# Kernel tuning notes

Hardware: AMD Instinct MI355X
Metric: run time of the kernel (lower is better)

Reference implementation:

```python
import jax, jax.numpy as jnp
import numpy as np

BETA_THRESH = 0.1   # threshold fraction in forward
BETA_IPOT = 0.5     # IPOT entropic beta
ITERATION = 30


def setup_inputs() -> dict:
    key = jax.random.key(0)
    k1, k2 = jax.random.split(key)
    bs, n, m, d = 64, 512, 512, 768
    return {
        "local_features_1": jax.random.normal(k1, (bs, n, d), dtype=jnp.float32),
        "local_features_2": jax.random.normal(k2, (bs, m, d), dtype=jnp.float32),
    }


def _wasserstein_loss(x, y):
    # x: (bs, n, d), y: (bs, m, d)
    # cost_matrix_batch_torch normalizes over the feature dim (dim=1 of bs*d*n layout)
    xn = x / (jnp.linalg.norm(x, axis=2, keepdims=True) + 1e-12)
    yn = y / (jnp.linalg.norm(y, axis=2, keepdims=True) + 1e-12)
    # cost_matrix returns (1 - cos).transpose(2,1); forward transposes back -> (bs, n, m)
    cos_distance = 1.0 - jnp.einsum("bnd,bmd->bnm", xn, yn)
    # global min/max threshold + relu
    min_score = cos_distance.min()
    max_score = cos_distance.max()
    threshold = min_score + BETA_THRESH * (max_score - min_score)
    C = jax.nn.relu(cos_distance - threshold)  # (bs, n, m)
    bs, n, m = C.shape
    A = jnp.exp(-C / BETA_IPOT)
    T0 = jnp.ones((bs, n, m), dtype=C.dtype)
    sigma0 = jnp.full((bs, m, 1), 1.0 / m, dtype=C.dtype)

    def step(carry, _):
        T, sigma = carry
        Q = A * T                                      # (bs, n, m)
        delta = 1.0 / (n * jnp.matmul(Q, sigma))       # (bs, n, 1)
        a = jnp.matmul(jnp.swapaxes(Q, 1, 2), delta)   # (bs, m, 1)
        sigma = 1.0 / (m * a)                          # (bs, m, 1)
        T = delta * Q * jnp.swapaxes(sigma, 1, 2)      # (bs, n, m)
        return (T, sigma), None

    (T, _), _ = jax.lax.scan(step, (T0, sigma0), None, length=ITERATION)
    # batch_trace(C^T @ T) == sum_ij C_ij * T_ij per batch element
    distance = jnp.einsum("bnm,bnm->b", C, T)
    # IPOT_distance returns -distance; loss is its mean
    return (-distance).mean()


def reference(local_features_1, local_features_2):
    return _wasserstein_loss(local_features_1, local_features_2)
```

## Files before the change

kernel.cpp:

```cpp
#include <hip/hip_runtime.h>
#include <hip/hip_fp16.h>

#define NN 512
#define DD 768

typedef _Float16 half8 __attribute__((ext_vector_type(8)));
typedef _Float16 half4 __attribute__((ext_vector_type(4)));
typedef _Float16 half2v __attribute__((ext_vector_type(2)));
typedef float f32x4 __attribute__((ext_vector_type(4)));

__device__ __forceinline__ int f2ord(float f) {
  int i = __float_as_int(f);
  return i < 0 ? (i ^ 0x7fffffff) : i;
}
__device__ __forceinline__ float ord2f(int i) {
  return __int_as_float(i < 0 ? (i ^ 0x7fffffff) : i);
}

__device__ __forceinline__ void glds16(const void* g, void* l) {
  __builtin_amdgcn_global_load_lds((const __attribute__((address_space(1))) void*)g,
                                   (__attribute__((address_space(3))) void*)l, 16, 0, 0);
}

__global__ void k_init(int* meta, int* cnt) {
  int t = threadIdx.x;
  if (t == 0) {
    meta[0] = 0x7fffffff;
    meta[1] = 0x80000000;
    cnt[1024] = 0;
  }
  if (t < 64) cnt[t * 16] = 0;
}

__global__ __launch_bounds__(256) void k_norm(const float* __restrict__ f1,
                                              const float* __restrict__ f2,
                                              __half* __restrict__ xn,
                                              __half* __restrict__ yn) {
  int row = blockIdx.x * 4 + (threadIdx.x >> 6);
  int lane = threadIdx.x & 63;
  int r = row & 32767;
  const float* src = (row < 32768 ? f1 : f2) + (size_t)r * DD;
  __half* dst = (row < 32768 ? xn : yn) + (size_t)r * DD;
  f32x4 v0 = *(const f32x4*)(src + lane * 4);
  f32x4 v1 = *(const f32x4*)(src + lane * 4 + 256);
  f32x4 v2 = *(const f32x4*)(src + lane * 4 + 512);
  float s = v0[0]*v0[0] + v0[1]*v0[1] + v0[2]*v0[2] + v0[3]*v0[3]
          + v1[0]*v1[0] + v1[1]*v1[1] + v1[2]*v1[2] + v1[3]*v1[3]
          + v2[0]*v2[0] + v2[1]*v2[1] + v2[2]*v2[2] + v2[3]*v2[3];
  #pragma unroll
  for (int m = 1; m < 64; m <<= 1) s += __shfl_xor(s, m, 64);
  float f = 1.0f / (sqrtf(s) + 1e-12f);
  union U { __half2 h2[2]; uint2 u; };
  U u0, u1, u2;
  u0.h2[0] = __floats2half2_rn(v0[0]*f, v0[1]*f); u0.h2[1] = __floats2half2_rn(v0[2]*f, v0[3]*f);
  u1.h2[0] = __floats2half2_rn(v1[0]*f, v1[1]*f); u1.h2[1] = __floats2half2_rn(v1[2]*f, v1[3]*f);
  u2.h2[0] = __floats2half2_rn(v2[0]*f, v2[1]*f); u2.h2[1] = __floats2half2_rn(v2[2]*f, v2[3]*f);
  *(uint2*)(dst + lane * 4)       = u0.u;
  *(uint2*)(dst + lane * 4 + 256) = u1.u;
  *(uint2*)(dst + lane * 4 + 512) = u2.u;
}

#define FOR16(X) X(0) X(1) X(2) X(3) X(4) X(5) X(6) X(7) X(8) X(9) X(10) X(11) X(12) X(13) X(14) X(15)

#define AGLD(p) __hip_atomic_load((p), __ATOMIC_RELAXED, __HIP_MEMORY_SCOPE_AGENT)
#define AGST(p, v) __hip_atomic_store((p), (v), __ATOMIC_RELAXED, __HIP_MEMORY_SCOPE_AGENT)

struct IpotLds {
  float xs[128];
  float ys[NN];
  _Float16 zs[NN];
  _Float16 csh[8][520];
  float wred[8];
};
union MainLds {
  _Float16 Bs[2][16384];
  _Float16 At[4][8192];
  float mm[16];
  int mmi[16];
  IpotLds ip;
};

__global__ __launch_bounds__(512, 2) void k_main(const __half* __restrict__ xn,
                                                 const __half* __restrict__ yn,
                                                 int* __restrict__ meta,
                                                 int* __restrict__ cnt,
                                                 int* __restrict__ gmm,
                                                 float* __restrict__ gpart,
                                                 float* __restrict__ gdist) {
  __shared__ __align__(16) MainLds u;
  const int blk = blockIdx.x;
  const int b = blk & 63, qq = blk >> 6;
  const int tid = threadIdx.x;
  const int sv = tid >> 6, lane = tid & 63;
  const int fr = lane & 15;
  const int g8 = (lane >> 4) * 8;
  const int r0 = sv * 16;
  const int c0 = lane * 8;
  const __half* xnb = xn + ((size_t)b * NN + qq * 128 + sv * 16) * DD;
  const __half* ynb = yn + (size_t)b * NN * DD;

  f32x4 acc[32] = {};
#define STAGE(bf, kk) { \
    const __half* ys_ = ynb + (size_t)(sv * 64 + lane) * DD + (kk); \
    glds16(ys_ +  0, (char*)u.Bs[bf] +     sv * 1024); \
    glds16(ys_ +  8, (char*)u.Bs[bf] +  8192 + sv * 1024); \
    glds16(ys_ + 16, (char*)u.Bs[bf] + 16384 + sv * 1024); \
    glds16(ys_ + 24, (char*)u.Bs[bf] + 24576 + sv * 1024); }
  int buf = 0;
  STAGE(0, 0)
  half8 afp = *(const half8*)(xnb + (size_t)fr * DD + g8);
  for (int kk = 0; kk < DD; kk += 32) {
    __syncthreads();
    if (kk + 32 < DD) STAGE(buf ^ 1, kk + 32)
    half8 afc = afp;
    if (kk + 32 < DD) afp = *(const half8*)(xnb + (size_t)fr * DD + (kk + 32) + g8);
    #pragma unroll
    for (int c = 0; c < 32; ++c) {
      half8 bf = *(const half8*)(&u.Bs[buf][(lane >> 4) * 4096 + (16 * c + fr) * 8]);
      acc[c] = __builtin_amdgcn_mfma_f32_16x16x32_f16(afc, bf, acc[c], 0, 0, 0);
    }
    buf ^= 1;
  }

  float vmin = 1e30f, vmax = -1e30f;
  #pragma unroll
  for (int c = 0; c < 32; ++c) {
    #pragma unroll
    for (int r2 = 0; r2 < 4; ++r2) {
      float val = 1.0f - acc[c][r2];
      vmin = fminf(vmin, val); vmax = fmaxf(vmax, val);
    }
  }
  #pragma unroll
  for (int m = 1; m < 64; m <<= 1) {
    vmin = fminf(vmin, __shfl_xor(vmin, m, 64));
    vmax = fmaxf(vmax, __shfl_xor(vmax, m, 64));
  }
  __syncthreads();
  if (lane == 0) { u.mm[sv] = vmin; u.mm[8 + sv] = vmax; }
  __syncthreads();
  if (tid == 0) {
    float bm = u.mm[0], bx = u.mm[8];
    #pragma unroll
    for (int g = 1; g < 8; ++g) { bm = fminf(bm, u.mm[g]); bx = fmaxf(bx, u.mm[8 + g]); }
    AGST(gmm + blk, f2ord(bm));
    AGST(gmm + 256 + blk, f2ord(bx));
  }
  __syncthreads();
  if (tid == 0) {
    int* cnt2 = cnt + 1024;
    __hip_atomic_fetch_add(cnt2, 1, __ATOMIC_RELAXED, __HIP_MEMORY_SCOPE_AGENT);
    while (AGLD(cnt2) < 256) __builtin_amdgcn_s_sleep(1);
  }
  __syncthreads();
  {
    int mo = AGLD(gmm + tid);
    #pragma unroll
    for (int m = 1; m < 64; m <<= 1) {
      int o = __shfl_xor(mo, m, 64);
      mo = (sv < 4) ? (mo < o ? mo : o) : (mo > o ? mo : o);
    }
    if (lane == 0) u.mmi[sv] = mo;
  }
  __syncthreads();
  int gmnord = u.mmi[0], gmxord = u.mmi[4];
  #pragma unroll
  for (int g = 1; g < 4; ++g) {
    gmnord = gmnord < u.mmi[g] ? gmnord : u.mmi[g];
    gmxord = gmxord > u.mmi[4 + g] ? gmxord : u.mmi[4 + g];
  }
  const float gmn = ord2f(gmnord);
  const float gmx = ord2f(gmxord);
  const float thr = gmn + 0.1f * (gmx - gmn);

#define DECLAM(r) half8 A##r, M##r;
  FOR16(DECLAM)

#define TWRITE { \
    _Float16* reg_ = u.At[sv & 3]; \
    const int q_ = lane >> 4; \
    _Pragma("unroll") \
    for (int c = 0; c < 32; ++c) { \
      _Pragma("unroll") \
      for (int r2 = 0; r2 < 4; ++r2) { \
        float val_ = 1.0f - acc[c][r2]; \
        float a_ = __expf(-2.0f * fmaxf(val_ - thr, 0.0f)); \
        int off_ = (((4 * q_ + r2) * 1024 + (16 * c + fr) * 2) ^ (q_ << 4)) >> 1; \
        reg_[off_] = (_Float16)a_; \
      } \
    } }

#define TREAD(r) { \
    A##r = *(const half8*)((const char*)u.At[sv & 3] + \
            (((r) * 1024 + lane * 16) ^ ((((r) >> 2) & 3) << 4))); \
    M##r = A##r; }

  __syncthreads();
  if (sv < 4) TWRITE
  __syncthreads();
  if (sv < 4) { FOR16(TREAD) }
  __syncthreads();
  if (sv >= 4) TWRITE
  __syncthreads();
  if (sv >= 4) { FOR16(TREAD) }
  __syncthreads();

  if (tid < 256) *(half2v*)(u.ip.zs + 2 * tid) = (half2v){(_Float16)1.0f, (_Float16)1.0f};
  u.ip.ys[tid] = 1.0f;
  __syncthreads();

  int* mycnt = cnt + b * 16;

  #pragma unroll 1
  for (int t = 1; t <= 30; ++t) {
    half8 zv = *(const half8*)(u.ip.zs + c0);
    float rp16[16];
#define ROWP(r) { \
      half8 p = M##r * zv; \
      half4 q = p.lo + p.hi; \
      half2v q2 = q.lo + q.hi; \
      rp16[r] = (float)q2.x + (float)q2.y; }
    FOR16(ROWP)
    float c8[8];
    #pragma unroll
    for (int i = 0; i < 8; ++i) {
      float keep = (lane & 1) ? rp16[2*i+1] : rp16[2*i];
      float send = (lane & 1) ? rp16[2*i]   : rp16[2*i+1];
      c8[i] = keep + __shfl_xor(send, 1, 64);
    }
    float c4[4];
    #pragma unroll
    for (int i = 0; i < 4; ++i) {
      float keep = (lane & 2) ? c8[2*i+1] : c8[2*i];
      float send = (lane & 2) ? c8[2*i]   : c8[2*i+1];
      c4[i] = keep + __shfl_xor(send, 2, 64);
    }
    float d2[2];
    #pragma unroll
    for (int i = 0; i < 2; ++i) {
      float keep = (lane & 4) ? c4[2*i+1] : c4[2*i];
      float send = (lane & 4) ? c4[2*i]   : c4[2*i+1];
      d2[i] = keep + __shfl_xor(send, 4, 64);
    }
    float c1;
    {
      float keep = (lane & 8) ? d2[1] : d2[0];
      float send = (lane & 8) ? d2[0] : d2[1];
      c1 = keep + __shfl_xor(send, 8, 64);
    }
    c1 += __shfl_xor(c1, 16, 64);
    c1 += __shfl_xor(c1, 32, 64);
    if (lane < 16) u.ip.xs[r0 + lane] = 1.0f / c1;
    half8 cac = (half8)(_Float16)0.0f;
#define COLP(r) { _Float16 xh = (_Float16)u.ip.xs[r0 + r]; cac += M##r * xh; }
    FOR16(COLP)
    *(half8*)(&u.ip.csh[sv][c0]) = cac;
#define UPDM(r) M##r *= A##r;
    if (t < 30) { FOR16(UPDM) }
    __syncthreads();
    float* gp = gpart + ((size_t)((t & 1) * 256 + blk) * 512);
    if (tid < 256) {
      float a0 = 0.0f, a1 = 0.0f;
      #pragma unroll
      for (int g = 0; g < 8; ++g) {
        half2v pv = *(const half2v*)(&u.ip.csh[g][2 * tid]);
        a0 += (float)pv.x; a1 += (float)pv.y;
      }
      AGST(gp + tid * 2,     a0);
      AGST(gp + tid * 2 + 1, a1);
    }
    __syncthreads();
    if (tid == 0) {
      __hip_atomic_fetch_add(mycnt, 1, __ATOMIC_RELAXED, __HIP_MEMORY_SCOPE_AGENT);
      while (__hip_atomic_load(mycnt, __ATOMIC_RELAXED, __HIP_MEMORY_SCOPE_AGENT) < 4 * t)
        __builtin_amdgcn_s_sleep(1);
    }
    __syncthreads();
    if (tid < 256) {
      float a0 = 0.0f, a1 = 0.0f;
      #pragma unroll
      for (int q2 = 0; q2 < 4; ++q2) {
        const float* gpb = gpart + ((size_t)((t & 1) * 256 + b + 64 * q2) * 512);
        a0 += AGLD(gpb + tid * 2);
        a1 += AGLD(gpb + tid * 2 + 1);
      }
      float yo0 = u.ip.ys[2 * tid], yo1 = u.ip.ys[2 * tid + 1];
      float y0 = 1.0f / a0;
      float y1 = 1.0f / a1;
      *(half2v*)(u.ip.zs + 2 * tid) = (half2v){(_Float16)(y0 * y0 / yo0), (_Float16)(y1 * y1 / yo1)};
      u.ip.ys[2 * tid] = y0; u.ip.ys[2 * tid + 1] = y1;
    }
    __syncthreads();
  }

  float contrib = 0.0f;
#define FINP(r) { \
    float rowacc = 0.0f; \
    rowacc += -0.34657359f * __log2f((float)A##r.s0) * (float)M##r.s0 * u.ip.ys[c0 + 0]; \
    rowacc += -0.34657359f * __log2f((float)A##r.s1) * (float)M##r.s1 * u.ip.ys[c0 + 1]; \
    rowacc += -0.34657359f * __log2f((float)A##r.s2) * (float)M##r.s2 * u.ip.ys[c0 + 2]; \
    rowacc += -0.34657359f * __log2f((float)A##r.s3) * (float)M##r.s3 * u.ip.ys[c0 + 3]; \
    rowacc += -0.34657359f * __log2f((float)A##r.s4) * (float)M##r.s4 * u.ip.ys[c0 + 4]; \
    rowacc += -0.34657359f * __log2f((float)A##r.s5) * (float)M##r.s5 * u.ip.ys[c0 + 5]; \
    rowacc += -0.34657359f * __log2f((float)A##r.s6) * (float)M##r.s6 * u.ip.ys[c0 + 6]; \
    rowacc += -0.34657359f * __log2f((float)A##r.s7) * (float)M##r.s7 * u.ip.ys[c0 + 7]; \
    contrib += rowacc * u.ip.xs[r0 + r]; }
  FOR16(FINP)
  #pragma unroll
  for (int m = 1; m < 64; m <<= 1) contrib += __shfl_xor(contrib, m, 64);
  if (lane == 0) u.ip.wred[sv] = contrib;
  __syncthreads();
  if (tid == 0) {
    float s2 = 0.0f;
    #pragma unroll
    for (int g = 0; g < 8; ++g) s2 += u.ip.wred[g];
    gdist[blk] = s2;
  }
}

__global__ void k_final(const float* __restrict__ gdist, float* __restrict__ out) {
  int b = threadIdx.x & 63;
  float v = gdist[b] + gdist[b + 64] + gdist[b + 128] + gdist[b + 192];
  #pragma unroll
  for (int m = 1; m < 64; m <<= 1) v += __shfl_xor(v, m, 64);
  if (threadIdx.x == 0) out[0] = -v * (1.0f / (64.0f * 512.0f));
}

extern "C" void kernel_launch(void* const* d_in, const int* in_sizes, int n_in,
                              void* d_out, int out_size, void* d_ws, size_t ws_size,
                              hipStream_t stream) {
  const float* f1 = (const float*)d_in[0];
  const float* f2 = (const float*)d_in[1];
  char* ws = (char*)d_ws;
  __half* xn   = (__half*)(ws + 0);
  __half* yn   = (__half*)(ws + 50331648);
  float* gpart = (float*)(ws + 100663296);
  int*   meta  = (int*)(ws + 167772160);
  int*   cnt   = (int*)(ws + 167772160 + 256);
  int*   gmm   = (int*)(ws + 167772160 + 256 + 8192);
  float* gdist = (float*)(ws + 167772160 + 256 + 8192 + 2048);

  k_init<<<1, 64, 0, stream>>>(meta, cnt);
  k_norm<<<16384, 256, 0, stream>>>(f1, f2, xn, yn);
  k_main<<<256, 512, 0, stream>>>(xn, yn, meta, cnt, gmm, gpart, gdist);
  k_final<<<1, 64, 0, stream>>>(gdist, (float*)d_out);
}
```

Baseline: 227.0 us.

## Pack cross-block IPOT partial sums as half2 and coalesce B-tile staging

The per-iteration cross-block column partial sums are now stored in global memory as packed half2 words instead of two floats, halving the traffic exchanged between cooperating blocks on each of the 30 IPOT iterations. The Y-tile staging into LDS is reorganized so that groups of four lanes read contiguous 64-byte row segments, and the LDS fragment indexing changes to match. The spin-wait loop now uses an explicit atomic load. Rounding partial sums to fp16 before the reciprocal adds precision loss to the sigma update.

```diff
diff --git a/kernel.cpp b/kernel.cpp
--- a/kernel.cpp
+++ b/kernel.cpp
@@ -85,7 +85,7 @@
                                                  int* __restrict__ meta,
                                                  int* __restrict__ cnt,
                                                  int* __restrict__ gmm,
-                                                 float* __restrict__ gpart,
+                                                 unsigned* __restrict__ gpart,
                                                  float* __restrict__ gdist) {
   __shared__ __align__(16) MainLds u;
   const int blk = blockIdx.x;
@@ -101,11 +101,11 @@
 
   f32x4 acc[32] = {};
 #define STAGE(bf, kk) { \
-    const __half* ys_ = ynb + (size_t)(sv * 64 + lane) * DD + (kk); \
-    glds16(ys_ +  0, (char*)u.Bs[bf] +     sv * 1024); \
-    glds16(ys_ +  8, (char*)u.Bs[bf] +  8192 + sv * 1024); \
-    glds16(ys_ + 16, (char*)u.Bs[bf] + 16384 + sv * 1024); \
-    glds16(ys_ + 24, (char*)u.Bs[bf] + 24576 + sv * 1024); }
+    _Pragma("unroll") \
+    for (int j = 0; j < 4; ++j) { \
+      const __half* ys_ = ynb + (size_t)(128 * j + sv * 16 + (lane >> 2)) * DD + (kk) + (lane & 3) * 8; \
+      glds16(ys_, (char*)u.Bs[bf] + j * 8192 + sv * 1024); \
+    } }
   int buf = 0;
   STAGE(0, 0)
   half8 afp = *(const half8*)(xnb + (size_t)fr * DD + g8);
@@ -116,7 +116,7 @@
     if (kk + 32 < DD) afp = *(const half8*)(xnb + (size_t)fr * DD + (kk + 32) + g8);
     #pragma unroll
     for (int c = 0; c < 32; ++c) {
-      half8 bf = *(const half8*)(&u.Bs[buf][(lane >> 4) * 4096 + (16 * c + fr) * 8]);
+      half8 bf = *(const half8*)(&u.Bs[buf][(16 * c + fr) * 32 + g8]);
       acc[c] = __builtin_amdgcn_mfma_f32_16x16x32_f16(afc, bf, acc[c], 0, 0, 0);
     }
     buf ^= 1;
@@ -143,18 +143,19 @@
     float bm = u.mm[0], bx = u.mm[8];
     #pragma unroll
     for (int g = 1; g < 8; ++g) { bm = fminf(bm, u.mm[g]); bx = fmaxf(bx, u.mm[8 + g]); }
-    AGST(gmm + blk, f2ord(bm));
-    AGST(gmm + 256 + blk, f2ord(bx));
+    AGST(gmm + blk, (unsigned)f2ord(bm));
+    AGST(gmm + 256 + blk, (unsigned)f2ord(bx));
   }
   __syncthreads();
   if (tid == 0) {
     int* cnt2 = cnt + 1024;
     __hip_atomic_fetch_add(cnt2, 1, __ATOMIC_RELAXED, __HIP_MEMORY_SCOPE_AGENT);
-    while (AGLD(cnt2) < 256) __builtin_amdgcn_s_sleep(1);
+    while (__hip_atomic_load(cnt2, __ATOMIC_RELAXED, __HIP_MEMORY_SCOPE_AGENT) < 256)
+      __builtin_amdgcn_s_sleep(1);
   }
   __syncthreads();
   {
-    int mo = AGLD(gmm + tid);
+    int mo = (int)AGLD(gmm + tid);
     #pragma unroll
     for (int m = 1; m < 64; m <<= 1) {
       int o = __shfl_xor(mo, m, 64);
@@ -258,7 +259,7 @@
 #define UPDM(r) M##r *= A##r;
     if (t < 30) { FOR16(UPDM) }
     __syncthreads();
-    float* gp = gpart + ((size_t)((t & 1) * 256 + blk) * 512);
+    unsigned* gp = gpart + ((size_t)((t & 1) * 256 + blk) * 256);
     if (tid < 256) {
       float a0 = 0.0f, a1 = 0.0f;
       #pragma unroll
@@ -266,8 +267,8 @@
         half2v pv = *(const half2v*)(&u.ip.csh[g][2 * tid]);
         a0 += (float)pv.x; a1 += (float)pv.y;
       }
-      AGST(gp + tid * 2,     a0);
-      AGST(gp + tid * 2 + 1, a1);
+      __half2 ph = __floats2half2_rn(a0, a1);
+      AGST(gp + tid, *reinterpret_cast<unsigned*>(&ph));
     }
     __syncthreads();
     if (tid == 0) {
@@ -280,9 +281,10 @@
       float a0 = 0.0f, a1 = 0.0f;
       #pragma unroll
       for (int q2 = 0; q2 < 4; ++q2) {
-        const float* gpb = gpart + ((size_t)((t & 1) * 256 + b + 64 * q2) * 512);
-        a0 += AGLD(gpb + tid * 2);
-        a1 += AGLD(gpb + tid * 2 + 1);
+        unsigned v = AGLD(gpart + ((size_t)((t & 1) * 256 + b + 64 * q2) * 256) + tid);
+        __half2 h = *reinterpret_cast<__half2*>(&v);
+        float2 fv = __half22float2(h);
+        a0 += fv.x; a1 += fv.y;
       }
       float yo0 = u.ip.ys[2 * tid], yo1 = u.ip.ys[2 * tid + 1];
       float y0 = 1.0f / a0;
@@ -334,7 +336,7 @@
   char* ws = (char*)d_ws;
   __half* xn   = (__half*)(ws + 0);
   __half* yn   = (__half*)(ws + 50331648);
-  float* gpart = (float*)(ws + 100663296);
+  unsigned* gpart = (unsigned*)(ws + 100663296);
   int*   meta  = (int*)(ws + 167772160);
   int*   cnt   = (int*)(ws + 167772160 + 256);
   int*   gmm   = (int*)(ws + 167772160 + 256 + 8192);
@@ -342,6 +344,6 @@
 
   k_init<<<1, 64, 0, stream>>>(meta, cnt);
   k_norm<<<16384, 256, 0, stream>>>(f1, f2, xn, yn);
-  k_main<<<256, 512, 0, stream>>>(xn, yn, meta, cnt, gmm, gpart, gdist);
+  k_main<<<256, 512, 0, stream>>>(xn, yn, meta, cnt, (int*)gmm, gpart, gdist);
   k_final<<<1, 64, 0, stream>>>(gdist, (float*)d_out);
 }
```

New measurement: 196.6 us. -13.4%, faster.
